# Kernel optimization log

Measured on AMD Instinct MI355X. Metric: run time of the kernel, lower is better.

Reference implementation:

```python
import jax, jax.numpy as jnp
import numpy as np
import math

C, H, W = 3, 4096, 4096
B = 8            # block_size
K = 16           # keep_coeffs
COEFF_SCALE = 1.0
NH, NW = H // B, W // B
N = C * NH * NW * K  # total_params = 12_582_912


def _zigzag_indices(b):
    idx = []
    for s in range(2 * b - 1):
        if s % 2 == 0:
            for i in range(s + 1):
                j = s - i
                if i < b and j < b:
                    idx.append((i, j))
        else:
            for j in range(s + 1):
                i = s - j
                if i < b and j < b:
                    idx.append((i, j))
    return idx


def _flat_indices():
    # ptr ordering in torch sample(): c outer, then bh, bw, then zig-zag coeff
    zz = np.asarray(_zigzag_indices(B)[:K], dtype=np.int64)  # (K, 2)
    c = np.arange(C)[:, None, None, None]
    bh = np.arange(NH)[None, :, None, None]
    bw = np.arange(NW)[None, None, :, None]
    u = zz[:, 0][None, None, None, :]
    v = zz[:, 1][None, None, None, :]
    flat = c * (H * W) + (bh * B + u) * W + (bw * B + v)  # (C, NH, NW, K)
    return flat.reshape(-1).astype(np.int32)


def setup_inputs() -> dict:
    key = jax.random.key(0)
    k1, k2 = jax.random.split(key)
    mean = jax.random.normal(k1, (N,), dtype=jnp.float32)
    log_std = jnp.full((N,), -4.0, dtype=jnp.float32)
    eps = jax.random.normal(k2, (N,), dtype=jnp.float32)
    flat_idx = jnp.asarray(_flat_indices())
    return {"mean": mean, "log_std": log_std, "eps": eps, "flat_idx": flat_idx}


def reference(mean, log_std, eps, flat_idx):
    std = jnp.exp(log_std)
    sample = (mean + std * eps) * COEFF_SCALE  # (N,)
    # single vectorized scatter (indices are disjoint by construction)
    coeffs = jnp.zeros((C * H * W,), dtype=jnp.float32).at[flat_idx].set(
        sample, unique_indices=True).reshape(C, H, W)
    log2pi = math.log(2.0 * math.pi)
    log_prob = -0.5 * jnp.sum(eps * eps + 2.0 * log_std + log2pi)
    entropy = jnp.sum(0.5 * (1.0 + log2pi) + log_std)
    return coeffs, log_prob, entropy
```

## Files before the change

### kernel.cpp

```cpp
#include <hip/hip_runtime.h>


constexpr int W = 4096;
constexpr int H = 4096;
constexpr long long CHW = 3LL * 4096 * 4096;
constexpr float LOG2PI = 1.8378770664093453f;
constexpr int NBLK = 3072;
constexpr float NTOT = 12582912.0f;

__device__ __constant__ unsigned long long RT[8] = {
    0xFFFFFF0A09030200ull,
    0xFFFFFFFF0B080401ull,
    0xFFFFFFFFFF0C0705ull,
    0xFFFFFFFFFFFF0D06ull,
    0xFFFFFFFFFFFFFF0Eull,
    0xFFFFFFFFFFFFFF0Full,
    0xFFFFFFFFFFFFFFFFull,
    0xFFFFFFFFFFFFFFFFull
};

__global__ __launch_bounds__(256) void dct_policy_kernel(
    const float* __restrict__ mean,
    const float* __restrict__ log_std,
    const float* __restrict__ eps,
    float* __restrict__ out,
    float2* __restrict__ partials)
{
    __shared__ float smp[4][64 * 17];
    __shared__ float p1[4], p2[4];

    const int t   = threadIdx.x;
    const int bid = blockIdx.x;
    const int c   = bid >> 10;
    const int rem = bid & 1023;
    const int bh  = rem >> 1;
    const int hx  = rem & 1;

    const long long pbase = (long long)(c * 512 + bh) * 8192 + (long long)hx * 4096;

    float4 m4[4], l4[4], e4[4];
#pragma unroll
    for (int k = 0; k < 4; ++k) {
        const long long g = pbase + k * 1024 + 4 * t;
        m4[k] = *(const float4*)(mean    + g);
        l4[k] = *(const float4*)(log_std + g);
        e4[k] = *(const float4*)(eps     + g);
    }

    const int tile = t >> 2;
    const int rb   = (t & 3) * 4;
    float s1 = 0.f, s2 = 0.f;
#pragma unroll
    for (int k = 0; k < 4; ++k) {
        const float mv[4] = {m4[k].x, m4[k].y, m4[k].z, m4[k].w};
        const float lv[4] = {l4[k].x, l4[k].y, l4[k].z, l4[k].w};
        const float ev[4] = {e4[k].x, e4[k].y, e4[k].z, e4[k].w};
#pragma unroll
        for (int j = 0; j < 4; ++j) {
            const float s = mv[j] + __builtin_expf(lv[j]) * ev[j];
            smp[k][tile * 17 + rb + j] = s;
            s1 += ev[j] * ev[j];
            s2 += lv[j];
        }
    }

#pragma unroll
    for (int off = 32; off > 0; off >>= 1) {
        s1 += __shfl_xor(s1, off, 64);
        s2 += __shfl_xor(s2, off, 64);
    }
    if ((t & 63) == 0) { p1[t >> 6] = s1; p2[t >> 6] = s2; }

    __syncthreads();

    if (t == 0) {
        partials[bid] = make_float2(p1[0] + p1[1] + p1[2] + p1[3],
                                    p2[0] + p2[1] + p2[2] + p2[3]);
    }

    const long long obase = (long long)c * ((long long)H * W)
                          + (long long)(bh * 8) * W + (long long)hx * 2048;
#pragma unroll
    for (int k = 0; k < 4; ++k) {
        const long long ob = obase + k * 512;
#pragma unroll
        for (int q = 0; q < 4; ++q) {
            const int f    = t + 256 * q;
            const int u    = f >> 7;
            const int x4   = f & 127;
            const int tl   = x4 >> 1;
            const int vb   = (x4 & 1) * 4;
            const unsigned long long row = RT[u];
            float4 o;
            float* ov = (float*)&o;
#pragma unroll
            for (int j = 0; j < 4; ++j) {
                const unsigned r = (unsigned)((row >> (8 * (vb + j))) & 0xFFull);
                const float v = smp[k][tl * 17 + (int)(r & 15u)];
                ov[j] = (r != 0xFFu) ? v : 0.0f;
            }
            *(float4*)(out + ob + (long long)u * W + x4 * 4) = o;
        }
    }
}

__global__ __launch_bounds__(256) void reduce_kernel(
    const float2* __restrict__ partials,
    float* __restrict__ out)
{
    const int t = threadIdx.x;
    float s1 = 0.f, s2 = 0.f;
    for (int i = t; i < NBLK; i += 256) {
        const float2 v = partials[i];
        s1 += v.x;
        s2 += v.y;
    }
#pragma unroll
    for (int off = 32; off > 0; off >>= 1) {
        s1 += __shfl_xor(s1, off, 64);
        s2 += __shfl_xor(s2, off, 64);
    }
    __shared__ float a1[4], a2[4];
    if ((t & 63) == 0) { a1[t >> 6] = s1; a2[t >> 6] = s2; }
    __syncthreads();
    if (t == 0) {
        const float S1 = a1[0] + a1[1] + a1[2] + a1[3];
        const float S2 = a2[0] + a2[1] + a2[2] + a2[3];
        out[CHW]     = -0.5f * S1 - S2 - 0.5f * NTOT * LOG2PI;
        out[CHW + 1] = 0.5f * (1.0f + LOG2PI) * NTOT + S2;
    }
}

extern "C" void kernel_launch(void* const* d_in, const int* in_sizes, int n_in,
                              void* d_out, int out_size, void* d_ws, size_t ws_size,
                              hipStream_t stream) {
    const float* mean    = (const float*)d_in[0];
    const float* log_std = (const float*)d_in[1];
    const float* eps     = (const float*)d_in[2];
    float* out = (float*)d_out;
    float2* partials = (float2*)d_ws;

    dct_policy_kernel<<<NBLK, 256, 0, stream>>>(mean, log_std, eps, out, partials);
    reduce_kernel<<<1, 256, 0, stream>>>(partials, out);
}
```

Measured before the change: 336.9 us.

## Give each wavefront its own LDS slice and drop the barrier before stores

Each wavefront now loads, computes and writes its own 512-column chunk through a private shared-memory slice. The output stores can then start before the block-wide barrier, which is kept only for the final partial-sum write. The zigzag lookup moves from a constant-memory 64-bit table to a compile-time table, so zero-only output columns skip the LDS read entirely. This gives up cross-wave sharing and changes the global load pattern to per-wave contiguous 1 KB chunks.

```diff
diff --git a/kernel.cpp b/kernel.cpp
--- a/kernel.cpp
+++ b/kernel.cpp
@@ -8,15 +8,15 @@
 constexpr int NBLK = 3072;
 constexpr float NTOT = 12582912.0f;
 
-__device__ __constant__ unsigned long long RT[8] = {
-    0xFFFFFF0A09030200ull,
-    0xFFFFFFFF0B080401ull,
-    0xFFFFFFFFFF0C0705ull,
-    0xFFFFFFFFFFFF0D06ull,
-    0xFFFFFFFFFFFFFF0Eull,
-    0xFFFFFFFFFFFFFF0Full,
-    0xFFFFFFFFFFFFFFFFull,
-    0xFFFFFFFFFFFFFFFFull
+constexpr unsigned char ZR[8][8] = {
+    {0,    2,    3,    9,    10,   0xFF, 0xFF, 0xFF},
+    {1,    4,    8,    11,   0xFF, 0xFF, 0xFF, 0xFF},
+    {5,    7,    12,   0xFF, 0xFF, 0xFF, 0xFF, 0xFF},
+    {6,    13,   0xFF, 0xFF, 0xFF, 0xFF, 0xFF, 0xFF},
+    {14,   0xFF, 0xFF, 0xFF, 0xFF, 0xFF, 0xFF, 0xFF},
+    {15,   0xFF, 0xFF, 0xFF, 0xFF, 0xFF, 0xFF, 0xFF},
+    {0xFF, 0xFF, 0xFF, 0xFF, 0xFF, 0xFF, 0xFF, 0xFF},
+    {0xFF, 0xFF, 0xFF, 0xFF, 0xFF, 0xFF, 0xFF, 0xFF}
 };
 
 __global__ __launch_bounds__(256) void dct_policy_kernel(
@@ -30,37 +30,41 @@
     __shared__ float p1[4], p2[4];
 
     const int t   = threadIdx.x;
+    const int w   = t >> 6;
+    const int ln  = t & 63;
     const int bid = blockIdx.x;
     const int c   = bid >> 10;
     const int rem = bid & 1023;
     const int bh  = rem >> 1;
     const int hx  = rem & 1;
 
-    const long long pbase = (long long)(c * 512 + bh) * 8192 + (long long)hx * 4096;
+    const long long pbase = (long long)(c * 512 + bh) * 8192
+                          + (long long)hx * 4096 + (long long)w * 1024;
 
     float4 m4[4], l4[4], e4[4];
 #pragma unroll
-    for (int k = 0; k < 4; ++k) {
-        const long long g = pbase + k * 1024 + 4 * t;
-        m4[k] = *(const float4*)(mean    + g);
-        l4[k] = *(const float4*)(log_std + g);
-        e4[k] = *(const float4*)(eps     + g);
+    for (int j = 0; j < 4; ++j) {
+        const long long g = pbase + 256 * j + 4 * ln;
+        m4[j] = *(const float4*)(mean    + g);
+        l4[j] = *(const float4*)(log_std + g);
+        e4[j] = *(const float4*)(eps     + g);
     }
 
-    const int tile = t >> 2;
-    const int rb   = (t & 3) * 4;
+    const int g0 = ln >> 2;
+    const int rb = (ln & 3) * 4;
     float s1 = 0.f, s2 = 0.f;
 #pragma unroll
-    for (int k = 0; k < 4; ++k) {
-        const float mv[4] = {m4[k].x, m4[k].y, m4[k].z, m4[k].w};
-        const float lv[4] = {l4[k].x, l4[k].y, l4[k].z, l4[k].w};
-        const float ev[4] = {e4[k].x, e4[k].y, e4[k].z, e4[k].w};
+    for (int j = 0; j < 4; ++j) {
+        const int tile = 16 * j + g0;
+        const float mv[4] = {m4[j].x, m4[j].y, m4[j].z, m4[j].w};
+        const float lv[4] = {l4[j].x, l4[j].y, l4[j].z, l4[j].w};
+        const float ev[4] = {e4[j].x, e4[j].y, e4[j].z, e4[j].w};
 #pragma unroll
-        for (int j = 0; j < 4; ++j) {
-            const float s = mv[j] + __builtin_expf(lv[j]) * ev[j];
-            smp[k][tile * 17 + rb + j] = s;
-            s1 += ev[j] * ev[j];
-            s2 += lv[j];
+        for (int i = 0; i < 4; ++i) {
+            const float s = mv[i] + __builtin_expf(lv[i]) * ev[i];
+            smp[w][tile * 17 + rb + i] = s;
+            s1 += ev[i] * ev[i];
+            s2 += lv[i];
         }
     }
 
@@ -69,38 +73,38 @@
         s1 += __shfl_xor(s1, off, 64);
         s2 += __shfl_xor(s2, off, 64);
     }
-    if ((t & 63) == 0) { p1[t >> 6] = s1; p2[t >> 6] = s2; }
+    if (ln == 0) { p1[w] = s1; p2[w] = s2; }
+
+    const long long obase = (long long)c * ((long long)H * W)
+                          + (long long)(bh * 8) * W
+                          + (long long)hx * 2048 + (long long)w * 512;
+    const int par = ln & 1;
+#pragma unroll
+    for (int q = 0; q < 16; ++q) {
+        const int u  = q >> 1;
+        const int x4 = (q & 1) * 64 + ln;
+        const int tl = x4 >> 1;
+        float4 o;
+        float* ov = (float*)&o;
+#pragma unroll
+        for (int j = 0; j < 4; ++j) {
+            const int re = ZR[u][j];
+            const int ro = ZR[u][4 + j];
+            if (re == 0xFF && ro == 0xFF) {
+                ov[j] = 0.0f;
+            } else {
+                const int r = par ? ro : re;
+                const float v = smp[w][tl * 17 + (r & 15)];
+                ov[j] = (r != 0xFF) ? v : 0.0f;
+            }
+        }
+        *(float4*)(out + obase + (long long)u * W + (long long)x4 * 4) = o;
+    }
 
     __syncthreads();
-
     if (t == 0) {
         partials[bid] = make_float2(p1[0] + p1[1] + p1[2] + p1[3],
                                     p2[0] + p2[1] + p2[2] + p2[3]);
-    }
-
-    const long long obase = (long long)c * ((long long)H * W)
-                          + (long long)(bh * 8) * W + (long long)hx * 2048;
-#pragma unroll
-    for (int k = 0; k < 4; ++k) {
-        const long long ob = obase + k * 512;
-#pragma unroll
-        for (int q = 0; q < 4; ++q) {
-            const int f    = t + 256 * q;
-            const int u    = f >> 7;
-            const int x4   = f & 127;
-            const int tl   = x4 >> 1;
-            const int vb   = (x4 & 1) * 4;
-            const unsigned long long row = RT[u];
-            float4 o;
-            float* ov = (float*)&o;
-#pragma unroll
-            for (int j = 0; j < 4; ++j) {
-                const unsigned r = (unsigned)((row >> (8 * (vb + j))) & 0xFFull);
-                const float v = smp[k][tl * 17 + (int)(r & 15u)];
-                ov[j] = (r != 0xFFu) ? v : 0.0f;
-            }
-            *(float4*)(out + ob + (long long)u * W + x4 * 4) = o;
-        }
     }
 }
 
```

Result: no change. 335.6 us (-0.4%).
